# Optimization experiments

Hardware: AMD Instinct MI355X
Metric: run time of the kernel (lower is better)

Reference implementation:

```python
import jax, jax.numpy as jnp
import numpy as np
from jax import lax

B, DIM, H, W = 32, 64, 1, 8192
HEADS = 8
EPS_LN = 1e-5
EPS_NORM = 1e-12


def setup_inputs() -> dict:
    key = jax.random.key(0)
    ks = jax.random.split(key, 20)
    g = lambda i, shape, s=0.05: jax.random.normal(ks[i], shape, jnp.float32) * s
    return dict(
        x=jax.random.normal(ks[0], (B, DIM, H, W), jnp.float32),
        qkv_w=g(1, (3 * DIM, DIM)), qkv_b=g(2, (3 * DIM,)),
        dw_w=g(3, (3 * DIM, 1, 3, 3)), dw_b=g(4, (3 * DIM,)),
        proj_w=g(5, (DIM, DIM)), proj_b=g(6, (DIM,)),
        temperature=jnp.ones((HEADS, 1, 1), jnp.float32),
        sp_w=g(7, (DIM,)), sp_b=g(8, (1,)),
        up_w=g(9, (3,)), up_b=g(10, (3,)),
        c2_w=g(11, (1, 1, 2)), c2_b=g(11, (1,)), ln2_w=jnp.ones((W,), jnp.float32), ln2_b=jnp.zeros((W,), jnp.float32),
        c4_w=g(12, (1, 1, 4)), c4_b=g(13, (1,)), ln4_w=jnp.ones((W,), jnp.float32), ln4_b=jnp.zeros((W,), jnp.float32),
        c6_w=g(14, (1, 1, 6)), c6_b=g(15, (1,)), ln6_w=jnp.ones((W,), jnp.float32), ln6_b=jnp.zeros((W,), jnp.float32),
        mp_w=g(16, (DIM,)), mp_b=g(17, (DIM,)),
    )


def _mtl(xs, cw, cb, lw, lb):
    """Multiscale_Temporal_Layer: conv1d 'same' -> LayerNorm(W) -> ELU -> mean pool. xs: (b,1,w)."""
    k = cw.shape[-1]
    tot = k - 1
    lo = tot // 2  # torch 'same': extra pad goes to the right
    y = lax.conv_general_dilated(xs, cw, (1,), [(lo, tot - lo)],
                                 dimension_numbers=('NCH', 'OIH', 'NCH'))
    y = y + cb[None, :, None]
    mu = jnp.mean(y, -1, keepdims=True)
    var = jnp.mean((y - mu) ** 2, -1, keepdims=True)
    y = (y - mu) / jnp.sqrt(var + EPS_LN) * lw + lb
    y = jax.nn.elu(y)
    return jnp.mean(y, -1, keepdims=True)  # (b,1,1)


def _forward(x, qkv_w, qkv_b, dw_w, dw_b, proj_w, proj_b, temperature,
             sp_w, sp_b, up_w, up_b,
             c2_w, c2_b, ln2_w, ln2_b,
             c4_w, c4_b, ln4_w, ln4_b,
             c6_w, c6_b, ln6_w, ln6_b,
             mp_w, mp_b):
    b, c, h, w = x.shape
    hd = c // HEADS  # per-head channel dim
    # 1x1 conv qkv, then depthwise 3x3 conv
    qkv = jnp.einsum('oc,bchw->bohw', qkv_w, x) + qkv_b[None, :, None, None]
    qkv = lax.conv_general_dilated(qkv, dw_w, (1, 1), [(1, 1), (1, 1)],
                                   dimension_numbers=('NCHW', 'OIHW', 'NCHW'),
                                   feature_group_count=3 * c)
    qkv = qkv + dw_b[None, :, None, None]
    q, k, v = jnp.split(qkv, 3, axis=1)
    # Multiscale_Temporal_Attention on v: v is (b,c,1,w)
    xseq = (jnp.einsum('c,bcw->bw', sp_w, v[:, :, 0, :]) + sp_b)[:, None, :]  # (b,1,w)
    up = up_w[None, :, None] * xseq + up_b[None, :, None]  # (b,3,w)
    xx, yy, zz = up[:, 0:1], up[:, 1:2], up[:, 2:3]
    mout = (_mtl(xx, c2_w, c2_b, ln2_w, ln2_b) * xx
            + _mtl(yy, c4_w, c4_b, ln4_w, ln4_b) * yy
            + _mtl(zz, c6_w, c6_b, ln6_w, ln6_b) * zz)  # (b,1,w)
    v = mp_w[None, :, None] * mout + mp_b[None, :, None]  # (b,c,w) via 1x1 conv broadcast
    # channel (transposed) attention over n = h*w tokens
    n = h * w
    q = q.reshape(b, HEADS, hd, n)
    k = k.reshape(b, HEADS, hd, n)
    v = v.reshape(b, HEADS, hd, n)
    q = q / jnp.maximum(jnp.linalg.norm(q, axis=-1, keepdims=True), EPS_NORM)
    k = k / jnp.maximum(jnp.linalg.norm(k, axis=-1, keepdims=True), EPS_NORM)
    attn = jnp.einsum('bhcn,bhdn->bhcd', q, k) * temperature  # (b,heads,hd,hd)
    attn = jax.nn.softmax(attn, axis=-1)
    out = jnp.einsum('bhcd,bhdn->bhcn', attn, v).reshape(b, c, h, w)
    out = jnp.einsum('oc,bchw->bohw', proj_w, out) + proj_b[None, :, None, None]
    return out  # dropouts are identity in eval mode


def reference(x, qkv_w, qkv_b, dw_w, dw_b, proj_w, proj_b, temperature,
              sp_w, sp_b, up_w, up_b,
              c2_w, c2_b, ln2_w, ln2_b,
              c4_w, c4_b, ln4_w, ln4_b,
              c6_w, c6_b, ln6_w, ln6_b,
              mp_w, mp_b):
    return _forward(x, qkv_w, qkv_b, dw_w, dw_b, proj_w, proj_b, temperature,
                    sp_w, sp_b, up_w, up_b,
                    c2_w, c2_b, ln2_w, ln2_b,
                    c4_w, c4_b, ln4_w, ln4_b,
                    c6_w, c6_b, ln6_w, ln6_b,
                    mp_w, mp_b)
```

## Files before the change

kernel.cpp:

```cpp
#include <hip/hip_runtime.h>
#include <hip/hip_bf16.h>
#include <math.h>

#define Wd 8192
#define Bd 32
#define NCH 16

#define OFF_G    0
#define OFF_H    192
#define OFF_BASE 195
#define OFF_XSEQ 256
#define OFF_SXP  (OFF_XSEQ + Bd*Wd)
#define OFF_RX   (OFF_SXP + Bd*NCH*64)
#define OFF_T    (OFF_RX + Bd*NCH*12288)
#define OFF_VEC  (OFF_T + Bd*3*1152)
#define OFF_WM   (OFF_VEC + Bd*640)

typedef __attribute__((ext_vector_type(8))) short bf16x8;
typedef __attribute__((ext_vector_type(4))) float f32x4;

__device__ __forceinline__ unsigned short f2bf(float v) {
    return __builtin_bit_cast(unsigned short, __float2bfloat16(v));
}
__device__ __forceinline__ float bf2f(unsigned short h) {
    return __builtin_bit_cast(float, (unsigned)h << 16);
}

__global__ __launch_bounds__(256) void k0_setup(const float* __restrict__ qkv_w,
                         const float* __restrict__ qkv_b,
                         const float* __restrict__ dw_w, const float* __restrict__ dw_b,
                         const float* __restrict__ sp_w, const float* __restrict__ sp_b,
                         float* __restrict__ ws)
{
    __shared__ float sw[64*64];
    __shared__ float sdw[192];
    __shared__ float ssp[64], sqb[64], sdb[64];
    int tid = threadIdx.x;
    for (int i = tid; i < 4096; i += 256) sw[i] = qkv_w[128*64 + i];
    if (tid < 192) { int c = tid/3, j = tid - 3*c; sdw[tid] = dw_w[(128+c)*9 + 3 + j]; }
    if (tid < 64)  { ssp[tid] = sp_w[tid]; sqb[tid] = qkv_b[128+tid]; sdb[tid] = dw_b[128+tid]; }
    __syncthreads();
    if (tid < 192) {
        int j = tid >> 6, ch = tid & 63;
        float acc = 0.f;
        #pragma unroll 8
        for (int c = 0; c < 64; c++)
            acc += ssp[c] * sdw[c*3+j] * sw[c*64 + ch];
        ws[OFF_G + j*64 + ch] = acc;
    } else if (tid < 195) {
        int j = tid - 192;
        float h = 0.f;
        #pragma unroll 8
        for (int c = 0; c < 64; c++)
            h += ssp[c] * sdw[c*3+j] * sqb[c];
        ws[OFF_H + j] = h;
    } else if (tid == 195) {
        float base = sp_b[0];
        #pragma unroll 8
        for (int c = 0; c < 64; c++) base += ssp[c] * sdb[c];
        ws[OFF_BASE] = base;
    }
}

#define ROWB 576

__device__ __forceinline__ int swzoff(int row, int gr) {
    int s = (gr < 32) ? (gr ^ (row & 7)) : gr;
    return row*ROWB + s*16;
}

__device__ __forceinline__ void loadsub(const float* __restrict__ xbase, int p0,
                                        float4 pf[17]) {
    #pragma unroll
    for (int m = 0; m < 17; m++) {
        int F = threadIdx.x + 256*m;
        int row = F / 68, c4 = F - 68*row;
        int p = p0 - 8 + 4*c4;
        const float* src = xbase + (size_t)row*Wd + p;
        if ((unsigned)p <= (unsigned)(Wd-4)) {
            pf[m] = *(const float4*)src;
        } else {
            float4 v;
            v.x = ((unsigned)(p  ) < (unsigned)Wd) ? src[0] : 0.f;
            v.y = ((unsigned)(p+1) < (unsigned)Wd) ? src[1] : 0.f;
            v.z = ((unsigned)(p+2) < (unsigned)Wd) ? src[2] : 0.f;
            v.w = ((unsigned)(p+3) < (unsigned)Wd) ? src[3] : 0.f;
            pf[m] = v;
        }
    }
}
__device__ __forceinline__ void writesub(unsigned char* xb, const float4 pf[17]) {
    #pragma unroll
    for (int m = 0; m < 17; m++) {
        int F = threadIdx.x + 256*m;
        int row = F / 68, c4 = F - 68*row;
        uint2 wv;
        wv.x = (unsigned)f2bf(pf[m].x) | ((unsigned)f2bf(pf[m].y) << 16);
        wv.y = (unsigned)f2bf(pf[m].z) | ((unsigned)f2bf(pf[m].w) << 16);
        *(uint2*)(xb + swzoff(row, c4 >> 1) + (c4 & 1)*8) = wv;
    }
}

__global__ __launch_bounds__(256) void kR(const float* __restrict__ x,
                                          float* __restrict__ ws)
{
    __shared__ __align__(16) unsigned char xb[64*ROWB];
    __shared__ float phib[3][260];
    __shared__ float4 Gl[64];
    __shared__ float sxb[64][4];

    const int tid = threadIdx.x, lane = tid & 63, wv = tid >> 6;
    const int g = lane >> 4, lr = lane & 15;
    const int grp = blockIdx.x, b = blockIdx.y;
    const float* xbase = x + (size_t)b*64*Wd;

    if (tid < 64) Gl[tid] = (float4){ws[OFF_G+tid], ws[OFF_G+64+tid], ws[OFF_G+128+tid], 0.f};
    const float Hs0 = ws[OFF_H], Hs1 = ws[OFF_H+1], Hs2 = ws[OFF_H+2];
    const float base_ = ws[OFF_BASE];

    f32x4 a0[4], a1[4], a2[4];
    #pragma unroll
    for (int ct = 0; ct < 4; ct++) {
        a0[ct] = (f32x4){0,0,0,0}; a1[ct] = (f32x4){0,0,0,0}; a2[ct] = (f32x4){0,0,0,0};
    }
    float rs = 0.f;
    float4 pf[17];

    loadsub(xbase, grp*512, pf);
    writesub(xb, pf);
    __syncthreads();

    #pragma unroll
    for (int s = 0; s < 2; s++) {
        const int p0 = grp*512 + s*256;
        if (s == 0) loadsub(xbase, p0 + 256, pf);

        #pragma unroll
        for (int ks = 0; ks < 8; ks++) {
            int gr0 = 1 + 4*ks + g;
            bf16x8 A = *(const bf16x8*)(xb + swzoff(16*wv + lr, gr0));
            #pragma unroll
            for (int ct = 0; ct < 4; ct++) {
                int rb = 16*ct + lr;
                uint4 u = *(const uint4*)(xb + swzoff(rb, gr0));
                unsigned u4 = *(const unsigned*)(xb + swzoff(rb, gr0 + 1));
                uint4 v1 = { (u.x>>16)|(u.y<<16), (u.y>>16)|(u.z<<16),
                             (u.z>>16)|(u.w<<16), (u.w>>16)|(u4<<16) };
                uint4 v2 = { u.y, u.z, u.w, u4 };
                a0[ct] = __builtin_amdgcn_mfma_f32_16x16x32_bf16(A, __builtin_bit_cast(bf16x8,u),  a0[ct],0,0,0);
                a1[ct] = __builtin_amdgcn_mfma_f32_16x16x32_bf16(A, __builtin_bit_cast(bf16x8,v1), a1[ct],0,0,0);
                a2[ct] = __builtin_amdgcn_mfma_f32_16x16x32_bf16(A, __builtin_bit_cast(bf16x8,v2), a2[ct],0,0,0);
            }
        }
        for (int ci = tid; ci < 258; ci += 256) {
            int col = 7 + ci;
            int grc = col >> 3, off = (col & 7)*2;
            float f0 = 0.f, f1 = 0.f, f2 = 0.f;
            #pragma unroll 8
            for (int c = 0; c < 64; c++) {
                float xv = bf2f(*(const unsigned short*)(xb + swzoff(c, grc) + off));
                float4 gv = Gl[c];
                f0 += gv.x*xv; f1 += gv.y*xv; f2 += gv.z*xv;
            }
            phib[0][ci] = f0; phib[1][ci] = f1; phib[2][ci] = f2;
        }
        {
            int row = tid & 63, q = tid >> 6;
            float ssum = 0.f;
            #pragma unroll
            for (int i = 0; i < 8; i++) {
                uint4 u = *(const uint4*)(xb + swzoff(row, 1 + 8*q + i));
                ssum += (bf2f((unsigned short)u.x) + bf2f((unsigned short)(u.x>>16)))
                      + (bf2f((unsigned short)u.y) + bf2f((unsigned short)(u.y>>16)))
                      + (bf2f((unsigned short)u.z) + bf2f((unsigned short)(u.z>>16)))
                      + (bf2f((unsigned short)u.w) + bf2f((unsigned short)(u.w>>16)));
            }
            rs += ssum;
        }
        __syncthreads();
        {
            int w = p0 + tid;
            float v = base_ + Hs0 + Hs1 + Hs2
                    + phib[0][tid] + phib[1][tid+1] + phib[2][tid+2];
            if (w == 0) v -= Hs0;
            if (w == Wd-1) v -= Hs2;
            ws[OFF_XSEQ + (size_t)b*Wd + w] = v;
        }
        __syncthreads();
        if (s == 0) {
            writesub(xb, pf);
            __syncthreads();
        }
    }

    {
        float* pb = ws + OFF_RX + (size_t)(b*NCH + grp)*12288;
        #pragma unroll
        for (int ct = 0; ct < 4; ct++) {
            #pragma unroll
            for (int r = 0; r < 4; r++) {
                int c = 16*wv + 4*g + r, cc = 16*ct + lr;
                pb[        c*64 + cc] = a0[ct][r];
                pb[4096 +  c*64 + cc] = a1[ct][r];
                pb[8192 +  c*64 + cc] = a2[ct][r];
            }
        }
    }
    {
        int row = tid & 63, q = tid >> 6;
        sxb[row][q] = rs;
    }
    __syncthreads();
    if (tid < 64)
        ws[OFF_SXP + (size_t)(b*NCH + grp)*64 + tid] =
            (sxb[tid][0] + sxb[tid][1]) + (sxb[tid][2] + sxb[tid][3]);
}

#define KF_SW 0
#define KF_RX (128*68*4)
#define KF_NT (KF_RX + 64*68*4)
#define KF_SXR (KF_NT + 64*68*4)
#define KF_XC (KF_SXR + 64*4)
#define KF_BYTES (KF_XC + 256*4)

__device__ __forceinline__ float dot64p(const float* a, const float* b) {
    float s0=0.f,s1=0.f,s2=0.f,s3=0.f;
    #pragma unroll
    for (int k = 0; k < 64; k += 4) {
        float4 av = *(const float4*)(a+k), bv = *(const float4*)(b+k);
        s0 += av.x*bv.x; s1 += av.y*bv.y; s2 += av.z*bv.z; s3 += av.w*bv.w;
    }
    return (s0+s1)+(s2+s3);
}
__device__ __forceinline__ float blk_reduce_256(float v, float* sc) {
    #pragma unroll
    for (int off = 32; off > 0; off >>= 1) v += __shfl_down(v, off, 64);
    __syncthreads();
    if ((threadIdx.x & 63) == 0) sc[threadIdx.x >> 6] = v;
    __syncthreads();
    return sc[0] + sc[1] + sc[2] + sc[3];
}

__global__ __launch_bounds__(256) void kF(const float* __restrict__ x,
    const float* __restrict__ qkv_w,
    const float* __restrict__ up_w, const float* __restrict__ up_b,
    const float* __restrict__ c2_w, const float* __restrict__ c2_b,
    const float* __restrict__ ln2_w, const float* __restrict__ ln2_b,
    const float* __restrict__ c4_w, const float* __restrict__ c4_b,
    const float* __restrict__ ln4_w, const float* __restrict__ ln4_b,
    const float* __restrict__ c6_w, const float* __restrict__ c6_b,
    const float* __restrict__ ln6_w, const float* __restrict__ ln6_b,
    float* __restrict__ ws)
{
    __shared__ __align__(16) unsigned char sm[KF_BYTES];
    __shared__ float sc[4];
    const int tid = threadIdx.x, bx = blockIdx.x;

    if (bx < 96) {
        const int bb = bx / 3, d = bx - 3*bb;
        float* sW  = (float*)(sm + KF_SW);
        float* sRx = (float*)(sm + KF_RX);
        float* sNT = (float*)(sm + KF_NT);
        float* sxr = (float*)(sm + KF_SXR);
        float* xcol = (float*)(sm + KF_XC);

        #pragma unroll
        for (int k = 0; k < 8; k++) {
            int i4 = tid + 256*k;
            float4 v = ((const float4*)qkv_w)[i4];
            int r = i4 >> 4, c = (i4 & 15) << 2;
            *(float4*)(sW + r*68 + c) = v;
        }
        const float* rxp = ws + OFF_RX + (size_t)bb*NCH*12288 + d*4096;
        #pragma unroll
        for (int k = 0; k < 16; k++) {
            int idx = tid + 256*k;
            float s = 0.f;
            #pragma unroll
            for (int ch = 0; ch < NCH; ch++) s += rxp[(size_t)ch*12288 + idx];
            sRx[(idx>>6)*68 + (idx&63)] = s;
        }
        if (d == 0) {
            if (tid < 64) {
                float s = 0.f;
                #pragma unroll
                for (int ch = 0; ch < NCH; ch++) s += ws[OFF_SXP + (size_t)(bb*NCH+ch)*64 + tid];
                sxr[tid] = s;
            }
            {
                int c = tid & 63, v = tid >> 6;
                int colv = (v == 0) ? 0 : (v == 1) ? 1 : (v == 2) ? (Wd-2) : (Wd-1);
                xcol[v*64 + c] = x[((size_t)bb*64 + c)*Wd + colv];
            }
        }
        __syncthreads();
        if (d == 0 && tid < 128) {
            int r = tid;
            float Xi=0.f,x0=0.f,x1=0.f,xm2=0.f,xm1=0.f;
            #pragma unroll 8
            for (int c = 0; c < 64; c++) {
                float w = sW[r*68+c];
                Xi += w*sxr[c]; x0 += w*xcol[c]; x1 += w*xcol[64+c];
                xm2 += w*xcol[128+c]; xm1 += w*xcol[192+c];
            }
            float* vp = ws + OFF_VEC + bb*640;
            vp[r] = Xi; vp[128+r] = x0; vp[256+r] = x1; vp[384+r] = xm2; vp[512+r] = xm1;
        }
        {
            int ro = tid >> 4, co = tid & 15;
            float acc[4][4] = {};
            for (int k = 0; k < 64; k += 4) {
                float4 av[4], bv[4];
                #pragma unroll
                for (int i = 0; i < 4; i++) av[i] = *(const float4*)(sRx + (4*ro+i)*68 + k);
                #pragma unroll
                for (int j = 0; j < 4; j++) bv[j] = *(const float4*)(sW + (64+4*co+j)*68 + k);
                #pragma unroll
                for (int i = 0; i < 4; i++)
                    #pragma unroll
                    for (int j = 0; j < 4; j++)
                        acc[i][j] += av[i].x*bv[j].x + av[i].y*bv[j].y
                                   + av[i].z*bv[j].z + av[i].w*bv[j].w;
            }
            __syncthreads();
            #pragma unroll
            for (int i = 0; i < 4; i++)
                #pragma unroll
                for (int j = 0; j < 4; j++)
                    sNT[(4*co+j)*68 + 4*ro+i] = acc[i][j];
        }
        __syncthreads();
        float* Tp = ws + OFF_T + (size_t)(bb*3 + d)*1152;
        for (int e = tid; e < 512; e += 256) {
            int t = e >> 3, u = ((e>>6)<<3) + (e&7);
            Tp[e] = dot64p(sW + t*68, sNT + u*68);
        }
        if (tid < 64) Tp[1088 + tid] = dot64p(sW + (64+tid)*68, sNT + tid*68);
        __syncthreads();
        {
            int ro = tid >> 4, co = tid & 15;
            float acc[4][4] = {};
            for (int k = 0; k < 64; k += 4) {
                float4 av[4], bv[4];
                #pragma unroll
                for (int i = 0; i < 4; i++) av[i] = *(const float4*)(sRx + (4*ro+i)*68 + k);
                #pragma unroll
                for (int j = 0; j < 4; j++) bv[j] = *(const float4*)(sW + (4*co+j)*68 + k);
                #pragma unroll
                for (int i = 0; i < 4; i++)
                    #pragma unroll
                    for (int j = 0; j < 4; j++)
                        acc[i][j] += av[i].x*bv[j].x + av[i].y*bv[j].y
                                   + av[i].z*bv[j].z + av[i].w*bv[j].w;
            }
            __syncthreads();
            #pragma unroll
            for (int i = 0; i < 4; i++)
                #pragma unroll
                for (int j = 0; j < 4; j++)
                    sNT[(4*co+j)*68 + 4*ro+i] = acc[i][j];
        }
        __syncthreads();
        for (int e = tid; e < 512; e += 256) {
            int t = e >> 3, u = ((e>>6)<<3) + (e&7);
            Tp[512 + e] = dot64p(sW + (64+u)*68, sNT + t*68);
        }
        if (tid < 64) Tp[1024 + tid] = dot64p(sW + tid*68, sNT + tid*68);
        return;
    }

    int t2 = bx - 96;
    int br = t2 >> 5, b = t2 & 31;
    float* ys = (float*)sm;
    const float *cw, *lw, *lb; float cb; int K, lo;
    if (br == 0)      { cw = c2_w; cb = c2_b[0]; lw = ln2_w; lb = ln2_b; K = 2; lo = 0; }
    else if (br == 1) { cw = c4_w; cb = c4_b[0]; lw = ln4_w; lb = ln4_b; K = 4; lo = 1; }
    else              { cw = c6_w; cb = c6_b[0]; lw = ln6_w; lb = ln6_b; K = 6; lo = 2; }
    float uw = up_w[br], ub = up_b[br];
    const float* xr = ws + OFF_XSEQ + (size_t)b*Wd;

    float s = 0.f, s2 = 0.f;
    for (int w = tid; w < Wd; w += 256) {
        float y = cb;
        for (int m = 0; m < K; m++) {
            int p = w + m - lo;
            if (p >= 0 && p < Wd) y += cw[m] * (uw*xr[p] + ub);
        }
        ys[w] = y; s += y; s2 += y*y;
    }
    float mu = blk_reduce_256(s, sc) * (1.f/Wd);
    __syncthreads();
    float Ey2 = blk_reduce_256(s2, sc) * (1.f/Wd);
    float var = fmaxf(Ey2 - mu*mu, 0.f);
    float inv = 1.f / sqrtf(var + 1e-5f);
    float se = 0.f;
    for (int w = tid; w < Wd; w += 256) {
        float tt = (ys[w]-mu)*inv*lw[w] + lb[w];
        se += (tt > 0.f) ? tt : expm1f(tt);
    }
    float m = blk_reduce_256(se, sc) * (1.f/Wd);
    if (tid == 0) ws[OFF_WM + b*3 + br] = m;
}

__global__ __launch_bounds__(256) void k5_out(const float* __restrict__ ws,
    const float* __restrict__ qkv_b, const float* __restrict__ dw_w,
    const float* __restrict__ dw_b, const float* __restrict__ temperature,
    const float* __restrict__ mp_w, const float* __restrict__ mp_b,
    const float* __restrict__ up_w, const float* __restrict__ up_b,
    const float* __restrict__ proj_w, const float* __restrict__ proj_b,
    float* __restrict__ out)
{
    __shared__ float sT3[3][1152];
    __shared__ float vec[5][128];
    __shared__ float qb_[128], tb_[128], tp_[128][3];
    __shared__ float Sq[512], dgq[64], dgk[64];
    __shared__ float snk[64], sal[64], sbe[64], sE[64], sF[64];
    __shared__ float red[64][8];
    const int tid = threadIdx.x;
    const int chunk = blockIdx.x, b = blockIdx.y;

    for (int i = tid; i < 3456; i += 256) ((float*)sT3)[i] = ws[OFF_T + (size_t)b*3456 + i];
    for (int i = tid; i < 640; i += 256) ((float*)vec)[i] = ws[OFF_VEC + b*640 + i];
    if (tid < 128) {
        qb_[tid] = qkv_b[tid]; tb_[tid] = dw_b[tid];
        tp_[tid][0] = dw_w[tid*9+3]; tp_[tid][1] = dw_w[tid*9+4]; tp_[tid][2] = dw_w[tid*9+5];
    }
    __syncthreads();

    for (int ee = tid; ee < 640; ee += 256) {
        int r, s; float Tpv[3], Tmv[3];
        if (ee < 512) {
            r = ee >> 3; s = 64 + ((ee>>6)<<3) + (ee&7);
            #pragma unroll
            for (int d = 0; d < 3; d++) { Tpv[d] = sT3[d][ee]; Tmv[d] = sT3[d][512+ee]; }
        } else if (ee < 576) {
            r = s = ee - 512;
            #pragma unroll
            for (int d = 0; d < 3; d++) { Tpv[d] = Tmv[d] = sT3[d][1024 + r]; }
        } else {
            int u = ee - 576; r = s = 64 + u;
            #pragma unroll
            for (int d = 0; d < 3; d++) { Tpv[d] = Tmv[d] = sT3[d][1088 + u]; }
        }
        float Xr = vec[0][r], Xs = vec[0][s];
        float x0r = vec[1][r], x0s = vec[1][s];
        float x1r = vec[2][r], x1s = vec[2][s];
        float xm2r = vec[3][r], xm2s = vec[3][s];
        float xm1r = vec[4][r], xm1s = vec[4][s];
        float qr = qb_[r], qs = qb_[s];
        float C5[5];
        #pragma unroll
        for (int dd = 0; dd < 3; dd++) {
            float head_s = (dd>=1 ? x0s : 0.f) + (dd>=2 ? x1s : 0.f);
            float tail_r = (dd>=1 ? xm1r : 0.f) + (dd>=2 ? xm2r : 0.f);
            C5[2+dd] = Tpv[dd] + qr*(Xs - head_s) + qs*(Xr - tail_r) + (8192.f - dd)*qr*qs;
            float head_r = (dd>=1 ? x0r : 0.f) + (dd>=2 ? x1r : 0.f);
            float tail_s = (dd>=1 ? xm1s : 0.f) + (dd>=2 ? xm2s : 0.f);
            C5[2-dd] = Tmv[dd] + qs*(Xr - head_r) + qr*(Xs - tail_s) + (8192.f - dd)*qr*qs;
        }
        float y0r = x0r + qr, y0s = x0s + qs;
        float ym1r = xm1r + qr, ym1s = xm1s + qs;
        float Yr = Xr + 8192.f*qr, Ys = Xs + 8192.f*qs;
        float tbr = tb_[r], tbs = tb_[s];
        float G = 8192.f * tbr * tbs;
        float sumr = 0.f, sums = 0.f;
        #pragma unroll
        for (int i = 0; i < 3; i++) {
            sumr += tp_[r][i] * (Yr - (i==0 ? ym1r : 0.f) - (i==2 ? y0r : 0.f));
            sums += tp_[s][i] * (Ys - (i==0 ? ym1s : 0.f) - (i==2 ? y0s : 0.f));
        }
        G += tbr * sums + tbs * sumr;
        #pragma unroll
        for (int i = 0; i < 3; i++)
            #pragma unroll
            for (int j = 0; j < 3; j++) {
                float P = C5[2 + j - i];
                if (i == 2 && j == 2) P -= y0r * y0s;
                if (i == 0 && j == 0) P -= ym1r * ym1s;
                G += tp_[r][i] * tp_[s][j] * P;
            }
        if (ee < 512) Sq[ee] = G;
        else if (ee < 576) dgq[ee-512] = G;
        else dgk[ee-576] = G;
    }
    __syncthreads();

    float nq = 0.f;
    if (tid < 64) {
        nq = fmaxf(sqrtf(fmaxf(dgq[tid], 0.f)), 1e-12f);
        snk[tid] = fmaxf(sqrtf(fmaxf(dgk[tid], 0.f)), 1e-12f);
    }
    __syncthreads();
    if (tid < 64) {
        int h = tid >> 3;
        float temp = temperature[h];
        float lg[8], mx = -1e30f;
        #pragma unroll
        for (int d = 0; d < 8; d++) {
            lg[d] = Sq[tid*8 + d] / (nq * snk[h*8 + d]) * temp;
            mx = fmaxf(mx, lg[d]);
        }
        float sum = 0.f;
        #pragma unroll
        for (int d = 0; d < 8; d++) { lg[d] = expf(lg[d] - mx); sum += lg[d]; }
        float a = 0.f, bb2 = 0.f;
        #pragma unroll
        for (int d = 0; d < 8; d++) {
            float at = lg[d] / sum;
            a   += at * mp_w[h*8 + d];
            bb2 += at * mp_b[h*8 + d];
        }
        sal[tid] = a; sbe[tid] = bb2;
    }
    __syncthreads();
    {
        float m2 = ws[OFF_WM + b*3], m4 = ws[OFF_WM + b*3 + 1], m6 = ws[OFF_WM + b*3 + 2];
        float A_ = m2*up_w[0] + m4*up_w[1] + m6*up_w[2];
        float C_ = m2*up_b[0] + m4*up_b[1] + m6*up_b[2];
        int o = tid & 63, q = tid >> 6;
        float pa = 0.f, pb2 = 0.f;
        #pragma unroll
        for (int k = 0; k < 16; k++) {
            int c = 16*q + k;
            float pw = proj_w[o*64 + c];
            pa += pw * sal[c]; pb2 += pw * sbe[c];
        }
        red[o][q] = pa; red[o][4+q] = pb2;
        __syncthreads();
        if (tid < 64) {
            float Pa = (red[tid][0]+red[tid][1]) + (red[tid][2]+red[tid][3]);
            float Pb = (red[tid][4]+red[tid][5]) + (red[tid][6]+red[tid][7]);
            sE[tid] = A_ * Pa;
            sF[tid] = C_ * Pa + Pb + proj_b[tid];
        }
    }
    __syncthreads();
    const float4* xs4 = (const float4*)(ws + OFF_XSEQ + (size_t)b*Wd);
    float4 xv = xs4[chunk*128 + (tid & 127)];
    int oh = tid >> 7;
    float4* ob = (float4*)out + (size_t)b*64*2048 + chunk*128 + (tid & 127);
    #pragma unroll 8
    for (int oo = 0; oo < 32; oo++) {
        int o = oh*32 + oo;
        float e = sE[o], f = sF[o];
        float4 rr = { e*xv.x + f, e*xv.y + f, e*xv.z + f, e*xv.w + f };
        ob[(size_t)o*2048] = rr;
    }
}

extern "C" void kernel_launch(void* const* d_in, const int* in_sizes, int n_in,
                              void* d_out, int out_size, void* d_ws, size_t ws_size,
                              hipStream_t stream) {
    const float* x      = (const float*)d_in[0];
    const float* qkv_w  = (const float*)d_in[1];
    const float* qkv_b  = (const float*)d_in[2];
    const float* dw_w   = (const float*)d_in[3];
    const float* dw_b   = (const float*)d_in[4];
    const float* proj_w = (const float*)d_in[5];
    const float* proj_b = (const float*)d_in[6];
    const float* temperature = (const float*)d_in[7];
    const float* sp_w   = (const float*)d_in[8];
    const float* sp_b   = (const float*)d_in[9];
    const float* up_w   = (const float*)d_in[10];
    const float* up_b   = (const float*)d_in[11];
    const float* c2_w   = (const float*)d_in[12];
    const float* c2_b   = (const float*)d_in[13];
    const float* ln2_w  = (const float*)d_in[14];
    const float* ln2_b  = (const float*)d_in[15];
    const float* c4_w   = (const float*)d_in[16];
    const float* c4_b   = (const float*)d_in[17];
    const float* ln4_w  = (const float*)d_in[18];
    const float* ln4_b  = (const float*)d_in[19];
    const float* c6_w   = (const float*)d_in[20];
    const float* c6_b   = (const float*)d_in[21];
    const float* ln6_w  = (const float*)d_in[22];
    const float* ln6_b  = (const float*)d_in[23];
    const float* mp_w   = (const float*)d_in[24];
    const float* mp_b   = (const float*)d_in[25];
    float* ws  = (float*)d_ws;
    float* out = (float*)d_out;

    k0_setup<<<1, 256, 0, stream>>>(qkv_w, qkv_b, dw_w, dw_b, sp_w, sp_b, ws);
    kR<<<dim3(NCH, 32), 256, 0, stream>>>(x, ws);
    kF<<<192, 256, 0, stream>>>(x, qkv_w, up_w, up_b,
        c2_w, c2_b, ln2_w, ln2_b, c4_w, c4_b, ln4_w, ln4_b, c6_w, c6_b, ln6_w, ln6_b,
        ws);
    k5_out<<<dim3(16, 32), 256, 0, stream>>>(ws, qkv_b, dw_w, dw_b, temperature,
        mp_w, mp_b, up_w, up_b, proj_w, proj_b, out);
}
```

Baseline: 121.4 us.

## Split Gram and sequence-conv work into separate block roles of one kernel

The fused kR kernel, which computed the shifted MFMA Gram products, the 3-tap sequence projection and the row sums in one block, is replaced by kRX with twice as many blocks. The first 16 blocks per batch do only the MFMA Gram accumulation over a narrower tile with no left halo. The other 16 compute the sequence conv and row sums directly from global fp32 x using per-wave channel partial sums reduced through LDS. This is meant to raise parallelism and shorten the critical path per block, at the cost of reading x twice from global memory.

```diff
diff --git a/kernel.cpp b/kernel.cpp
--- a/kernel.cpp
+++ b/kernel.cpp
@@ -62,138 +62,87 @@
     }
 }
 
-#define ROWB 576
+#define ROWB 560
+#define SM_BYTES 35840
 
 __device__ __forceinline__ int swzoff(int row, int gr) {
     int s = (gr < 32) ? (gr ^ (row & 7)) : gr;
     return row*ROWB + s*16;
 }
 
-__device__ __forceinline__ void loadsub(const float* __restrict__ xbase, int p0,
-                                        float4 pf[17]) {
-    #pragma unroll
-    for (int m = 0; m < 17; m++) {
-        int F = threadIdx.x + 256*m;
-        int row = F / 68, c4 = F - 68*row;
-        int p = p0 - 8 + 4*c4;
-        const float* src = xbase + (size_t)row*Wd + p;
-        if ((unsigned)p <= (unsigned)(Wd-4)) {
-            pf[m] = *(const float4*)src;
-        } else {
-            float4 v;
-            v.x = ((unsigned)(p  ) < (unsigned)Wd) ? src[0] : 0.f;
-            v.y = ((unsigned)(p+1) < (unsigned)Wd) ? src[1] : 0.f;
-            v.z = ((unsigned)(p+2) < (unsigned)Wd) ? src[2] : 0.f;
-            v.w = ((unsigned)(p+3) < (unsigned)Wd) ? src[3] : 0.f;
-            pf[m] = v;
-        }
-    }
-}
-__device__ __forceinline__ void writesub(unsigned char* xb, const float4 pf[17]) {
-    #pragma unroll
-    for (int m = 0; m < 17; m++) {
-        int F = threadIdx.x + 256*m;
-        int row = F / 68, c4 = F - 68*row;
-        uint2 wv;
-        wv.x = (unsigned)f2bf(pf[m].x) | ((unsigned)f2bf(pf[m].y) << 16);
-        wv.y = (unsigned)f2bf(pf[m].z) | ((unsigned)f2bf(pf[m].w) << 16);
-        *(uint2*)(xb + swzoff(row, c4 >> 1) + (c4 & 1)*8) = wv;
-    }
-}
-
-__global__ __launch_bounds__(256) void kR(const float* __restrict__ x,
-                                          float* __restrict__ ws)
+__global__ __launch_bounds__(256) void kRX(const float* __restrict__ x,
+                                           float* __restrict__ ws)
 {
-    __shared__ __align__(16) unsigned char xb[64*ROWB];
-    __shared__ float phib[3][260];
-    __shared__ float4 Gl[64];
-    __shared__ float sxb[64][4];
-
+    __shared__ __align__(16) unsigned char sm[SM_BYTES];
     const int tid = threadIdx.x, lane = tid & 63, wv = tid >> 6;
-    const int g = lane >> 4, lr = lane & 15;
-    const int grp = blockIdx.x, b = blockIdx.y;
-    const float* xbase = x + (size_t)b*64*Wd;
-
-    if (tid < 64) Gl[tid] = (float4){ws[OFF_G+tid], ws[OFF_G+64+tid], ws[OFF_G+128+tid], 0.f};
-    const float Hs0 = ws[OFF_H], Hs1 = ws[OFF_H+1], Hs2 = ws[OFF_H+2];
-    const float base_ = ws[OFF_BASE];
-
-    f32x4 a0[4], a1[4], a2[4];
-    #pragma unroll
-    for (int ct = 0; ct < 4; ct++) {
-        a0[ct] = (f32x4){0,0,0,0}; a1[ct] = (f32x4){0,0,0,0}; a2[ct] = (f32x4){0,0,0,0};
-    }
-    float rs = 0.f;
-    float4 pf[17];
-
-    loadsub(xbase, grp*512, pf);
-    writesub(xb, pf);
-    __syncthreads();
-
-    #pragma unroll
-    for (int s = 0; s < 2; s++) {
-        const int p0 = grp*512 + s*256;
-        if (s == 0) loadsub(xbase, p0 + 256, pf);
-
-        #pragma unroll
-        for (int ks = 0; ks < 8; ks++) {
-            int gr0 = 1 + 4*ks + g;
-            bf16x8 A = *(const bf16x8*)(xb + swzoff(16*wv + lr, gr0));
-            #pragma unroll
-            for (int ct = 0; ct < 4; ct++) {
-                int rb = 16*ct + lr;
-                uint4 u = *(const uint4*)(xb + swzoff(rb, gr0));
-                unsigned u4 = *(const unsigned*)(xb + swzoff(rb, gr0 + 1));
-                uint4 v1 = { (u.x>>16)|(u.y<<16), (u.y>>16)|(u.z<<16),
-                             (u.z>>16)|(u.w<<16), (u.w>>16)|(u4<<16) };
-                uint4 v2 = { u.y, u.z, u.w, u4 };
-                a0[ct] = __builtin_amdgcn_mfma_f32_16x16x32_bf16(A, __builtin_bit_cast(bf16x8,u),  a0[ct],0,0,0);
-                a1[ct] = __builtin_amdgcn_mfma_f32_16x16x32_bf16(A, __builtin_bit_cast(bf16x8,v1), a1[ct],0,0,0);
-                a2[ct] = __builtin_amdgcn_mfma_f32_16x16x32_bf16(A, __builtin_bit_cast(bf16x8,v2), a2[ct],0,0,0);
-            }
-        }
-        for (int ci = tid; ci < 258; ci += 256) {
-            int col = 7 + ci;
-            int grc = col >> 3, off = (col & 7)*2;
-            float f0 = 0.f, f1 = 0.f, f2 = 0.f;
-            #pragma unroll 8
-            for (int c = 0; c < 64; c++) {
-                float xv = bf2f(*(const unsigned short*)(xb + swzoff(c, grc) + off));
-                float4 gv = Gl[c];
-                f0 += gv.x*xv; f1 += gv.y*xv; f2 += gv.z*xv;
-            }
-            phib[0][ci] = f0; phib[1][ci] = f1; phib[2][ci] = f2;
-        }
-        {
-            int row = tid & 63, q = tid >> 6;
-            float ssum = 0.f;
-            #pragma unroll
-            for (int i = 0; i < 8; i++) {
-                uint4 u = *(const uint4*)(xb + swzoff(row, 1 + 8*q + i));
-                ssum += (bf2f((unsigned short)u.x) + bf2f((unsigned short)(u.x>>16)))
-                      + (bf2f((unsigned short)u.y) + bf2f((unsigned short)(u.y>>16)))
-                      + (bf2f((unsigned short)u.z) + bf2f((unsigned short)(u.z>>16)))
-                      + (bf2f((unsigned short)u.w) + bf2f((unsigned short)(u.w>>16)));
-            }
-            rs += ssum;
-        }
-        __syncthreads();
-        {
-            int w = p0 + tid;
-            float v = base_ + Hs0 + Hs1 + Hs2
-                    + phib[0][tid] + phib[1][tid+1] + phib[2][tid+2];
-            if (w == 0) v -= Hs0;
-            if (w == Wd-1) v -= Hs2;
-            ws[OFF_XSEQ + (size_t)b*Wd + w] = v;
-        }
-        __syncthreads();
-        if (s == 0) {
-            writesub(xb, pf);
+    const int bx = blockIdx.x, b = blockIdx.y;
+
+    if (bx < 16) {
+        const int g = lane >> 4, lr = lane & 15;
+        const int grp = bx;
+        unsigned char* xb = sm;
+        f32x4 a0[4], a1[4], a2[4];
+        #pragma unroll
+        for (int ct = 0; ct < 4; ct++) {
+            a0[ct] = (f32x4){0,0,0,0}; a1[ct] = (f32x4){0,0,0,0}; a2[ct] = (f32x4){0,0,0,0};
+        }
+
+        #pragma unroll
+        for (int s = 0; s < 2; s++) {
+            const int p0 = grp*512 + s*256;
+            float4 pf[17];
+            #pragma unroll
+            for (int m = 0; m < 17; m++) {
+                int F = tid + 256*m;
+                if (F < 4224) {
+                    int row = F / 66, c4 = F - 66*row;
+                    int p = p0 + 4*c4;
+                    const float* src = x + ((size_t)b*64 + row)*Wd + p;
+                    if (p + 3 < Wd) {
+                        pf[m] = *(const float4*)src;
+                    } else {
+                        float4 v;
+                        v.x = (p   < Wd) ? src[0] : 0.f;
+                        v.y = (p+1 < Wd) ? src[1] : 0.f;
+                        v.z = (p+2 < Wd) ? src[2] : 0.f;
+                        v.w = (p+3 < Wd) ? src[3] : 0.f;
+                        pf[m] = v;
+                    }
+                }
+            }
+            if (s == 1) __syncthreads();
+            #pragma unroll
+            for (int m = 0; m < 17; m++) {
+                int F = tid + 256*m;
+                if (F < 4224) {
+                    int row = F / 66, c4 = F - 66*row;
+                    uint2 wvv;
+                    wvv.x = (unsigned)f2bf(pf[m].x) | ((unsigned)f2bf(pf[m].y) << 16);
+                    wvv.y = (unsigned)f2bf(pf[m].z) | ((unsigned)f2bf(pf[m].w) << 16);
+                    *(uint2*)(xb + swzoff(row, c4 >> 1) + (c4 & 1)*8) = wvv;
+                }
+            }
             __syncthreads();
-        }
-    }
-
-    {
+
+            #pragma unroll
+            for (int ks = 0; ks < 8; ks++) {
+                int gr0 = 4*ks + g;
+                bf16x8 A = *(const bf16x8*)(xb + swzoff(16*wv + lr, gr0));
+                #pragma unroll
+                for (int ct = 0; ct < 4; ct++) {
+                    int rb = 16*ct + lr;
+                    uint4 u = *(const uint4*)(xb + swzoff(rb, gr0));
+                    unsigned u4 = *(const unsigned*)(xb + swzoff(rb, gr0 + 1));
+                    uint4 v1 = { (u.x>>16)|(u.y<<16), (u.y>>16)|(u.z<<16),
+                                 (u.z>>16)|(u.w<<16), (u.w>>16)|(u4<<16) };
+                    uint4 v2 = { u.y, u.z, u.w, u4 };
+                    a0[ct] = __builtin_amdgcn_mfma_f32_16x16x32_bf16(A, __builtin_bit_cast(bf16x8,u),  a0[ct],0,0,0);
+                    a1[ct] = __builtin_amdgcn_mfma_f32_16x16x32_bf16(A, __builtin_bit_cast(bf16x8,v1), a1[ct],0,0,0);
+                    a2[ct] = __builtin_amdgcn_mfma_f32_16x16x32_bf16(A, __builtin_bit_cast(bf16x8,v2), a2[ct],0,0,0);
+                }
+            }
+        }
+
         float* pb = ws + OFF_RX + (size_t)(b*NCH + grp)*12288;
         #pragma unroll
         for (int ct = 0; ct < 4; ct++) {
@@ -205,15 +154,76 @@
                 pb[8192 +  c*64 + cc] = a2[ct][r];
             }
         }
-    }
+        return;
+    }
+
     {
-        int row = tid & 63, q = tid >> 6;
-        sxb[row][q] = rs;
-    }
-    __syncthreads();
-    if (tid < 64)
-        ws[OFF_SXP + (size_t)(b*NCH + grp)*64 + tid] =
-            (sxb[tid][0] + sxb[tid][1]) + (sxb[tid][2] + sxb[tid][3]);
+        const int grp = bx - 16;
+        const int p0g = grp * 512;
+        float* xpart = (float*)sm;
+        float* rsl   = (float*)(sm + 8192);
+        float* rred  = (float*)(sm + 8192 + 16640);
+        float* ldsG  = (float*)(sm + 8192 + 16640 + 1024);
+
+        if (tid < 192) {
+            int j = tid >> 6, ch = tid & 63;
+            ldsG[ch*3 + j] = ws[OFF_G + tid];
+        }
+        const float Hs0 = ws[OFF_H], Hs1 = ws[OFF_H+1], Hs2 = ws[OFF_H+2];
+        const float base_ = ws[OFF_BASE];
+        __syncthreads();
+
+        const int own = p0g + 8*lane;
+        float acc[8] = {0.f,0.f,0.f,0.f,0.f,0.f,0.f,0.f};
+        const float* xbbase = x + (size_t)b*64*Wd;
+        #pragma unroll
+        for (int chi = 0; chi < 16; ++chi) {
+            int ch = wv*16 + chi;
+            const float* xr = xbbase + (size_t)ch*Wd;
+            float4 A  = *(const float4*)(xr + own);
+            float4 Bv = *(const float4*)(xr + own + 4);
+            float xm = (own > 0)      ? xr[own-1] : 0.f;
+            float xp = (own + 8 < Wd) ? xr[own+8] : 0.f;
+            float g0 = ldsG[ch*3], g1 = ldsG[ch*3+1], g2 = ldsG[ch*3+2];
+            acc[0] += g0*xm   + g1*A.x  + g2*A.y;
+            acc[1] += g0*A.x  + g1*A.y  + g2*A.z;
+            acc[2] += g0*A.y  + g1*A.z  + g2*A.w;
+            acc[3] += g0*A.z  + g1*A.w  + g2*Bv.x;
+            acc[4] += g0*A.w  + g1*Bv.x + g2*Bv.y;
+            acc[5] += g0*Bv.x + g1*Bv.y + g2*Bv.z;
+            acc[6] += g0*Bv.y + g1*Bv.z + g2*Bv.w;
+            acc[7] += g0*Bv.z + g1*Bv.w + g2*xp;
+            rsl[ch*65 + lane] = ((A.x+A.y)+(A.z+A.w)) + ((Bv.x+Bv.y)+(Bv.z+Bv.w));
+        }
+        *(float4*)(xpart + wv*512 + 8*lane)     = (float4){acc[0],acc[1],acc[2],acc[3]};
+        *(float4*)(xpart + wv*512 + 8*lane + 4) = (float4){acc[4],acc[5],acc[6],acc[7]};
+        __syncthreads();
+
+        {
+            int p = 2*tid;
+            float v0 = ((xpart[p]   + xpart[512+p])   + (xpart[1024+p]   + xpart[1536+p]));
+            float v1 = ((xpart[p+1] + xpart[512+p+1]) + (xpart[1024+p+1] + xpart[1536+p+1]));
+            int w = p0g + p;
+            float cst = base_ + Hs0 + Hs1 + Hs2;
+            float r0 = cst + v0;
+            float r1 = cst + v1;
+            if (w == 0) r0 -= Hs0;
+            if (w + 1 == Wd - 1) r1 -= Hs2;
+            *(float2*)(ws + OFF_XSEQ + (size_t)b*Wd + w) = (float2){r0, r1};
+        }
+        {
+            int ch = tid & 63, q = tid >> 6;
+            float s = 0.f;
+            #pragma unroll
+            for (int i = 0; i < 16; i++) s += rsl[ch*65 + q*16 + i];
+            rred[q*64 + ch] = s;
+        }
+        __syncthreads();
+        if (tid < 64) {
+            float t = (rred[tid] + rred[64+tid]) + (rred[128+tid] + rred[192+tid]);
+            ws[OFF_SXP + (size_t)(b*NCH + grp)*64 + tid] = t;
+        }
+    }
 }
 
 #define KF_SW 0
@@ -581,7 +591,7 @@
     float* out = (float*)d_out;
 
     k0_setup<<<1, 256, 0, stream>>>(qkv_w, qkv_b, dw_w, dw_b, sp_w, sp_b, ws);
-    kR<<<dim3(NCH, 32), 256, 0, stream>>>(x, ws);
+    kRX<<<dim3(32, 32), 256, 0, stream>>>(x, ws);
     kF<<<192, 256, 0, stream>>>(x, qkv_w, up_w, up_b,
         c2_w, c2_b, ln2_w, ln2_b, c4_w, c4_b, ln4_w, ln4_b, c6_w, c6_b, ln6_w, ln6_b,
         ws);
```

New measurement: 136.6 us, median of 3. 12.5% more time.
